# Optimization experiments

Hardware: AMD Instinct MI355X
Metric: run time of the kernel (lower is better)

## Reference

```python
import jax, jax.numpy as jnp
import numpy as np

B, L, D, M = 32, 512, 768, 24  # batch, max_len, bert hidden, mentions per sample
MAX_SPAN = 16


def setup_inputs() -> dict:
    key = jax.random.key(0)
    k1, k2, k3, k4 = jax.random.split(key, 4)
    sequence_output = jax.random.normal(k1, (B, L, D), dtype=jnp.float32)
    head_indexes = jax.random.randint(k2, (B, L), 0, L)
    starts = jax.random.randint(k3, (B, M), 0, L - MAX_SPAN)
    lens = jax.random.randint(k4, (B, M), 1, MAX_SPAN)
    entity_mentions = jnp.stack([starts, starts + lens], axis=-1)  # [B, M, 2], start < end
    return {
        "sequence_output": sequence_output,
        "head_indexes": head_indexes,
        "entity_mentions": entity_mentions,
    }


def reference(sequence_output, head_indexes, entity_mentions):
    b, l, d = sequence_output.shape
    m = entity_mentions.shape[1]

    # per-sample head-token gather: seq[i] = seq[i][head_indexes[i]]
    seq = jnp.take_along_axis(sequence_output, head_indexes[..., None], axis=1)  # [B, L, D]

    # span mean-pool via exclusive prefix sums: mean(seq[s:e]) = (cs[e]-cs[s])/(e-s)
    cs = jnp.concatenate(
        [jnp.zeros((b, 1, d), seq.dtype), jnp.cumsum(seq, axis=1)], axis=1
    )  # [B, L+1, D]
    starts = entity_mentions[..., 0]  # [B, M]
    ends = entity_mentions[..., 1]    # [B, M]
    span_sum = (
        jnp.take_along_axis(cs, ends[..., None], axis=1)
        - jnp.take_along_axis(cs, starts[..., None], axis=1)
    )  # [B, M, D]
    pooled = span_sum / (ends - starts)[..., None].astype(seq.dtype)  # [B, M, D]

    # all ordered pairs i != j (eval path order: i outer, j inner, skip i==j)
    ii, jj = np.meshgrid(np.arange(m), np.arange(m), indexing="ij")
    offdiag = ii != jj
    ii = jnp.asarray(ii[offdiag])  # [P]
    jj = jnp.asarray(jj[offdiag])  # [P]
    p = ii.shape[0]

    obj = pooled[:, ii]  # [B, P, D]
    sub = pooled[:, jj]  # [B, P, D]
    relation_predictions = jnp.concatenate([obj, sub], axis=-1).reshape(b * p, 2 * d)

    batch_idx = jnp.repeat(jnp.arange(b), p)  # [B*P]
    pairs = jnp.stack(
        [
            batch_idx,
            starts[:, ii].reshape(-1),
            ends[:, ii].reshape(-1),
            starts[:, jj].reshape(-1),
            ends[:, jj].reshape(-1),
        ],
        axis=-1,
    )  # [B*P, 5] = [idx, obj_start, obj_end, subj_start, subj_end]
    return relation_predictions, pairs
```

## Files before the change

### kernel.cpp

```cpp
#include <hip/hip_runtime.h>

#define B 32
#define L 512
#define D 768
#define M 24
#define P (M * (M - 1))
#define Q4 (D / 4)

typedef float f32x4 __attribute__((ext_vector_type(4)));

__global__ void __launch_bounds__(Q4)
pool_kernel(const float* __restrict__ seq,
            const int*   __restrict__ head,
            const int*   __restrict__ em,
            float*       __restrict__ pooled)
{
    int bm = blockIdx.x;
    int b = bm / M;
    int tq = threadIdx.x;

    int s = em[bm * 2 + 0];
    int e = em[bm * 2 + 1];
    int len = e - s;

    const float* seqb  = seq  + (size_t)b * L * D;
    const int*   headb = head + b * L;

    int hidx[15];
    #pragma unroll
    for (int r = 0; r < 15; ++r) {
        int l = s + r; l = (l < e) ? l : s;
        hidx[r] = headb[l];
    }
    f32x4 vv[15];
    #pragma unroll
    for (int r = 0; r < 15; ++r)
        vv[r] = ((const f32x4*)(seqb + (size_t)hidx[r] * D))[tq];
    f32x4 acc = (f32x4)(0.f);
    #pragma unroll
    for (int r = 0; r < 15; ++r)
        acc += (r < len) ? vv[r] : (f32x4)(0.f);
    acc *= 1.0f / (float)len;

    ((f32x4*)pooled)[(size_t)bm * Q4 + tq] = acc;
}

__global__ void __launch_bounds__(2 * Q4)
rel_kernel(const float* __restrict__ pooled,
           const int*   __restrict__ em,
           float*       __restrict__ out)
{
    int bp = blockIdx.x;
    int t  = threadIdx.x;
    int b  = bp / P;
    int p  = bp - b * P;
    int i  = p / (M - 1);
    int r  = p - i * (M - 1);
    int j  = (r < i) ? r : r + 1;

    int src_m = (t < Q4) ? i : j;
    int tq    = (t < Q4) ? t : t - Q4;
    f32x4 v = ((const f32x4*)pooled)[(size_t)(b * M + src_m) * Q4 + tq];
    __builtin_nontemporal_store(v, &((f32x4*)out)[(size_t)bp * 384 + t]);

    if (t == 0) {
        const int* emb = em + b * M * 2;
        float* o = out + (size_t)B * P * 2 * D + (size_t)bp * 5;
        o[0] = (float)b;
        o[1] = (float)emb[2 * i];
        o[2] = (float)emb[2 * i + 1];
        o[3] = (float)emb[2 * j];
        o[4] = (float)emb[2 * j + 1];
    }
}

extern "C" void kernel_launch(void* const* d_in, const int* in_sizes, int n_in,
                              void* d_out, int out_size, void* d_ws, size_t ws_size,
                              hipStream_t stream) {
    const float* seq  = (const float*)d_in[0];
    const int*   head = (const int*)d_in[1];
    const int*   em   = (const int*)d_in[2];
    float* out    = (float*)d_out;
    float* pooled = (float*)d_ws;

    pool_kernel<<<B * M, Q4, 0, stream>>>(seq, head, em, pooled);
    rel_kernel<<<B * P, 2 * Q4, 0, stream>>>(pooled, em, out);
}
```

Baseline: 30.33 us.

## Stage pooled mentions in LDS and write many pair rows per block

The relation kernel goes from one block per output pair row to one block per (batch, chunk). Each block copies that sample's 24 pooled vectors into shared memory and then loops over 69 pair rows, writing them from LDS. Pair metadata is now written by the pooling kernel, so the relation kernel no longer reads the mention indices. The stores also switch from nontemporal to plain stores. The goal is to cut per-block launch and scheduling overhead and repeated global reads, at the cost of only 256 blocks and a serial write loop per block, which may not keep HBM write bandwidth saturated.

```diff
diff --git a/kernel.cpp b/kernel.cpp
--- a/kernel.cpp
+++ b/kernel.cpp
@@ -6,6 +6,8 @@
 #define M 24
 #define P (M * (M - 1))
 #define Q4 (D / 4)
+#define CHUNKS 8
+#define ROWS_PER_BLK (P / CHUNKS)
 
 typedef float f32x4 __attribute__((ext_vector_type(4)));
 
@@ -13,10 +15,11 @@
 pool_kernel(const float* __restrict__ seq,
             const int*   __restrict__ head,
             const int*   __restrict__ em,
-            float*       __restrict__ pooled)
+            float*       __restrict__ pooled,
+            float*       __restrict__ pout)
 {
     int bm = blockIdx.x;
-    int b = bm / M;
+    int b = bm / M, m = bm - b * M;
     int tq = threadIdx.x;
 
     int s = em[bm * 2 + 0];
@@ -43,34 +46,51 @@
     acc *= 1.0f / (float)len;
 
     ((f32x4*)pooled)[(size_t)bm * Q4 + tq] = acc;
+
+    if (tq < 23) {
+        int r = tq;
+        int j = (r < m) ? r : r + 1;
+        const int* emb = em + b * M * 2;
+        float* o = pout + ((size_t)b * P + (size_t)m * 23 + r) * 5;
+        o[0] = (float)b;
+        o[1] = (float)s;
+        o[2] = (float)e;
+        o[3] = (float)emb[2 * j];
+        o[4] = (float)emb[2 * j + 1];
+    }
 }
 
 __global__ void __launch_bounds__(2 * Q4)
 rel_kernel(const float* __restrict__ pooled,
-           const int*   __restrict__ em,
            float*       __restrict__ out)
 {
-    int bp = blockIdx.x;
-    int t  = threadIdx.x;
-    int b  = bp / P;
-    int p  = bp - b * P;
-    int i  = p / (M - 1);
-    int r  = p - i * (M - 1);
-    int j  = (r < i) ? r : r + 1;
+    __shared__ f32x4 lpool[M * Q4];
 
-    int src_m = (t < Q4) ? i : j;
-    int tq    = (t < Q4) ? t : t - Q4;
-    f32x4 v = ((const f32x4*)pooled)[(size_t)(b * M + src_m) * Q4 + tq];
-    __builtin_nontemporal_store(v, &((f32x4*)out)[(size_t)bp * 384 + t]);
+    int blk   = blockIdx.x;
+    int b     = blk / CHUNKS;
+    int chunk = blk - b * CHUNKS;
+    int t     = threadIdx.x;
 
-    if (t == 0) {
-        const int* emb = em + b * M * 2;
-        float* o = out + (size_t)B * P * 2 * D + (size_t)bp * 5;
-        o[0] = (float)b;
-        o[1] = (float)emb[2 * i];
-        o[2] = (float)emb[2 * i + 1];
-        o[3] = (float)emb[2 * j];
-        o[4] = (float)emb[2 * j + 1];
+    const f32x4* src = (const f32x4*)pooled + (size_t)b * M * Q4;
+    #pragma unroll
+    for (int k = 0; k < M * Q4 / (2 * Q4); ++k)
+        lpool[k * 2 * Q4 + t] = src[k * 2 * Q4 + t];
+    __syncthreads();
+
+    int p0 = chunk * ROWS_PER_BLK;
+    int hf = t >= Q4;
+    int tq = hf ? t - Q4 : t;
+
+    f32x4* dst = (f32x4*)out + ((size_t)b * P + p0) * 384 + t;
+
+    for (int pr = 0; pr < ROWS_PER_BLK; ++pr) {
+        int p = p0 + pr;
+        int i = p / 23;
+        int r = p - i * 23;
+        int j = (r < i) ? r : r + 1;
+        int src_m = hf ? j : i;
+        *dst = lpool[src_m * Q4 + tq];
+        dst += 384;
     }
 }
 
@@ -83,6 +103,7 @@
     float* out    = (float*)d_out;
     float* pooled = (float*)d_ws;
 
-    pool_kernel<<<B * M, Q4, 0, stream>>>(seq, head, em, pooled);
-    rel_kernel<<<B * P, 2 * Q4, 0, stream>>>(pooled, em, out);
+    pool_kernel<<<B * M, Q4, 0, stream>>>(seq, head, em, pooled,
+                                          out + (size_t)B * P * 2 * D);
+    rel_kernel<<<B * CHUNKS, 2 * Q4, 0, stream>>>(pooled, out);
 }
```

Result: slower. 32.42 us (+6.9%).
